# Optimization experiments

Hardware: AMD Instinct MI355X
Metric: run time of the kernel (lower is better)

The kernel has to match this reference:

```python
import jax, jax.numpy as jnp
import numpy as np

N_QUBITS = 4
Q_DEPTH = 6
Q_DELTA = 0.01
INPUT_SIZE = 64
BATCH = 262144


def _ry_gate(theta):
    # RY(theta) = [[cos(t/2), -sin(t/2)], [sin(t/2), cos(t/2)]]; theta scalar or (B,)
    c = jnp.cos(theta / 2)
    s = jnp.sin(theta / 2)
    return jnp.stack([jnp.stack([c, -s], -1), jnp.stack([s, c], -1)], -2)


def _apply_1q(state, gate, wire):
    # state: (B,2,2,2,2); gate: (2,2) shared or (B,2,2) per-sample
    ax = wire + 1
    s = jnp.moveaxis(state, ax, -1)
    if gate.ndim == 2:
        s = jnp.einsum('ij,b...j->b...i', gate, s)
    else:
        s = jnp.einsum('bij,b...j->b...i', gate, s)
    return jnp.moveaxis(s, -1, ax)


def _apply_cnot(state, ctrl, tgt):
    ca, ta = ctrl + 1, tgt + 1
    s0 = jnp.take(state, jnp.array([0]), axis=ca)
    s1 = jnp.take(state, jnp.array([1]), axis=ca)
    s1 = jnp.flip(s1, axis=ta)  # X on target where control=1
    return jnp.concatenate([s0, s1], axis=ca)


def _quantum_net(q_in, q_weights):
    # q_in: (B, 4) per-sample RY angles; q_weights: (Q_DEPTH, 4)
    B = q_in.shape[0]
    # H layer on |0000>: uniform real amplitude 1/4 over all 16 basis states
    state = jnp.full((B,) + (2,) * N_QUBITS, 0.25, dtype=q_in.dtype)
    for w in range(N_QUBITS):
        state = _apply_1q(state, _ry_gate(q_in[:, w]), w)
    for k in range(Q_DEPTH):
        for i in range(0, N_QUBITS - 1, 2):
            state = _apply_cnot(state, i, i + 1)
        for i in range(1, N_QUBITS - 1, 2):
            state = _apply_cnot(state, i, i + 1)
        for w in range(N_QUBITS):
            state = _apply_1q(state, _ry_gate(q_weights[k, w]), w)
    # All gates are real -> real statevector; probs = amp^2
    probs = state * state
    signs = jnp.array([1.0, -1.0], dtype=state.dtype)
    expz = []
    for w in range(N_QUBITS):
        shp = [1] * (N_QUBITS + 1)
        shp[w + 1] = 2
        expz.append(jnp.sum(probs * signs.reshape(shp), axis=tuple(range(1, N_QUBITS + 1))))
    return jnp.stack(expz, axis=-1)  # (B, 4)


def setup_inputs() -> dict:
    key = jax.random.key(0)
    k1, k2, k3, k4, k5, k6 = jax.random.split(key, 6)
    bound_pre = 1.0 / np.sqrt(INPUT_SIZE)
    bound_post = 1.0 / np.sqrt(N_QUBITS)
    return {
        'input_features': jax.random.normal(k1, (BATCH, INPUT_SIZE), dtype=jnp.float32),
        'pre_w': jax.random.uniform(k2, (N_QUBITS, INPUT_SIZE), jnp.float32, -bound_pre, bound_pre),
        'pre_b': jax.random.uniform(k3, (N_QUBITS,), jnp.float32, -bound_pre, bound_pre),
        'q_params': Q_DELTA * jax.random.normal(k4, (Q_DEPTH * N_QUBITS,), dtype=jnp.float32),
        'post_w': jax.random.uniform(k5, (1, N_QUBITS), jnp.float32, -bound_post, bound_post),
        'post_b': jax.random.uniform(k6, (1,), jnp.float32, -bound_post, bound_post),
    }


def reference(input_features, pre_w, pre_b, q_params, post_w, post_b):
    pre_out = input_features @ pre_w.T + pre_b
    q_in = jnp.tanh(pre_out) * (jnp.pi / 2.0)
    q_out = _quantum_net(q_in, q_params.reshape(Q_DEPTH, N_QUBITS))
    return q_out @ post_w.T + post_b  # (B, 1)
```

## Files before the change

### kernel.cpp

```cpp
#include <hip/hip_runtime.h>
#include <math.h>

#define NQ      4
#define QDEPTH  6
#define TPB     128
#define ROWLEN  64
#define LSTRIDE 68

__device__ __forceinline__ float fast_tanh(float x) {
    float e = __expf(2.0f * x);
    float r = __builtin_amdgcn_rcpf(e + 1.0f);
    return fmaf(-2.0f, r, 1.0f);
}

template<int W>
__device__ __forceinline__ void apply_ry(float st[16], float c, float s) {
    constexpr int M = 8 >> W;
#pragma unroll
    for (int i = 0; i < 16; ++i) {
        if ((i & M) == 0) {
            float a0 = st[i];
            float a1 = st[i | M];
            st[i]     = fmaf(c, a0, -(s * a1));
            st[i | M] = fmaf(s, a0,  (c * a1));
        }
    }
}

template<int C, int T>
__device__ __forceinline__ void apply_cnot(float st[16]) {
    constexpr int MC = 8 >> C;
    constexpr int MT = 8 >> T;
#pragma unroll
    for (int i = 0; i < 16; ++i) {
        if ((i & MC) != 0 && (i & MT) == 0) {
            float tmp = st[i];
            st[i] = st[i | MT];
            st[i | MT] = tmp;
        }
    }
}

__global__ __launch_bounds__(TPB, 2) void dqnet_kernel(
    const float* __restrict__ inp,
    const float* __restrict__ pre_w,
    const float* __restrict__ pre_b,
    const float* __restrict__ qp,
    const float* __restrict__ post_w,
    const float* __restrict__ post_b,
    float* __restrict__ out)
{
    __shared__ float tile[TPB * LSTRIDE];
    __shared__ float cw[QDEPTH * NQ];
    __shared__ float sw[QDEPTH * NQ];
    __shared__ float gg[16];

    const int t = threadIdx.x;

    if (t < QDEPTH * NQ) {
        float h = 0.5f * qp[t];
        cw[t] = cosf(h);
        sw[t] = sinf(h);
    } else if (t >= 32 && t < 48) {
        int i = t - 32;
        float v = 0.0f;
#pragma unroll
        for (int w = 0; w < NQ; ++w) {
            float p = post_w[w];
            v += ((i >> (3 - w)) & 1) ? -p : p;
        }
        gg[i] = v;
    }

    const float4* in4 = (const float4*)(inp + (size_t)blockIdx.x * (TPB * ROWLEN));
#pragma unroll
    for (int j = 0; j < 16; ++j) {
        int f = j * TPB + t;
        float4 v = in4[f];
        int s  = f >> 4;
        int c4 = f & 15;
        *(float4*)&tile[s * LSTRIDE + 4 * c4] = v;
    }
    __syncthreads();

    float acc0 = pre_b[0], acc1 = pre_b[1], acc2 = pre_b[2], acc3 = pre_b[3];
    const float4* pw4 = (const float4*)pre_w;
#pragma unroll
    for (int i4 = 0; i4 < 16; ++i4) {
        float4 x  = *(const float4*)&tile[t * LSTRIDE + 4 * i4];
        float4 w0 = pw4[i4];
        float4 w1 = pw4[16 + i4];
        float4 w2 = pw4[32 + i4];
        float4 w3 = pw4[48 + i4];
        acc0 = fmaf(x.x, w0.x, acc0); acc0 = fmaf(x.y, w0.y, acc0);
        acc0 = fmaf(x.z, w0.z, acc0); acc0 = fmaf(x.w, w0.w, acc0);
        acc1 = fmaf(x.x, w1.x, acc1); acc1 = fmaf(x.y, w1.y, acc1);
        acc1 = fmaf(x.z, w1.z, acc1); acc1 = fmaf(x.w, w1.w, acc1);
        acc2 = fmaf(x.x, w2.x, acc2); acc2 = fmaf(x.y, w2.y, acc2);
        acc2 = fmaf(x.z, w2.z, acc2); acc2 = fmaf(x.w, w2.w, acc2);
        acc3 = fmaf(x.x, w3.x, acc3); acc3 = fmaf(x.y, w3.y, acc3);
        acc3 = fmaf(x.z, w3.z, acc3); acc3 = fmaf(x.w, w3.w, acc3);
    }

    const float QK = 0.78539816339744831f;
    float h0 = fast_tanh(acc0) * QK;
    float h1 = fast_tanh(acc1) * QK;
    float h2 = fast_tanh(acc2) * QK;
    float h3 = fast_tanh(acc3) * QK;
    float c0 = __cosf(h0), s0 = __sinf(h0);
    float c1 = __cosf(h1), s1 = __sinf(h1);
    float c2 = __cosf(h2), s2 = __sinf(h2);
    float c3 = __cosf(h3), s3 = __sinf(h3);

    const float R = 0.70710678118654752f;
    float u0 = (c0 - s0) * R, v0 = (c0 + s0) * R;
    float u1 = (c1 - s1) * R, v1 = (c1 + s1) * R;
    float u2 = (c2 - s2) * R, v2 = (c2 + s2) * R;
    float u3 = (c3 - s3) * R, v3 = (c3 + s3) * R;

    float p00 = u0 * u1, p01 = u0 * v1, p10 = v0 * u1, p11 = v0 * v1;
    float q00 = u2 * u3, q01 = u2 * v3, q10 = v2 * u3, q11 = v2 * v3;

    float st[16];
    st[ 0] = p00 * q00; st[ 1] = p00 * q01; st[ 2] = p00 * q10; st[ 3] = p00 * q11;
    st[ 4] = p01 * q00; st[ 5] = p01 * q01; st[ 6] = p01 * q10; st[ 7] = p01 * q11;
    st[ 8] = p10 * q00; st[ 9] = p10 * q01; st[10] = p10 * q10; st[11] = p10 * q11;
    st[12] = p11 * q00; st[13] = p11 * q01; st[14] = p11 * q10; st[15] = p11 * q11;

#pragma unroll
    for (int k = 0; k < QDEPTH; ++k) {
        apply_cnot<0, 1>(st);
        apply_cnot<2, 3>(st);
        apply_cnot<1, 2>(st);
        apply_ry<0>(st, cw[k * 4 + 0], sw[k * 4 + 0]);
        apply_ry<1>(st, cw[k * 4 + 1], sw[k * 4 + 1]);
        apply_ry<2>(st, cw[k * 4 + 2], sw[k * 4 + 2]);
        apply_ry<3>(st, cw[k * 4 + 3], sw[k * 4 + 3]);
    }

    float r = post_b[0];
#pragma unroll
    for (int i = 0; i < 16; ++i)
        r = fmaf(st[i] * st[i], gg[i], r);

    out[(size_t)blockIdx.x * TPB + t] = r;
}

extern "C" void kernel_launch(void* const* d_in, const int* in_sizes, int n_in,
                              void* d_out, int out_size, void* d_ws, size_t ws_size,
                              hipStream_t stream) {
    const float* inp    = (const float*)d_in[0];
    const float* pre_w  = (const float*)d_in[1];
    const float* pre_b  = (const float*)d_in[2];
    const float* qp     = (const float*)d_in[3];
    const float* post_w = (const float*)d_in[4];
    const float* post_b = (const float*)d_in[5];
    float* out = (float*)d_out;

    int n = in_sizes[0] / ROWLEN;
    int grid = n / TPB;
    dqnet_kernel<<<grid, TPB, 0, stream>>>(inp, pre_w, pre_b, qp, post_w, post_b, out);
}
```

Baseline: 103.9 us.

## Load input rows directly from global memory instead of staging through LDS

Drops the shared-memory tile that staged each block's input rows. Each thread now reads its own 256-byte row with float4 loads straight from global memory. Block size doubles to 256 and the launch bound asks for 4 blocks per CU, and the weight cos/sin moves to fast intrinsics. The aim is to remove LDS traffic and free the LDS limit on occupancy, at the cost of strided, uncoalesced per-thread loads across a wavefront that depend on cache-line reuse.

```diff
diff --git a/kernel.cpp b/kernel.cpp
--- a/kernel.cpp
+++ b/kernel.cpp
@@ -3,9 +3,8 @@
 
 #define NQ      4
 #define QDEPTH  6
-#define TPB     128
+#define TPB     256
 #define ROWLEN  64
-#define LSTRIDE 68
 
 __device__ __forceinline__ float fast_tanh(float x) {
     float e = __expf(2.0f * x);
@@ -41,7 +40,7 @@
     }
 }
 
-__global__ __launch_bounds__(TPB, 2) void dqnet_kernel(
+__global__ __launch_bounds__(TPB, 4) void dqnet_kernel(
     const float* __restrict__ inp,
     const float* __restrict__ pre_w,
     const float* __restrict__ pre_b,
@@ -50,7 +49,6 @@
     const float* __restrict__ post_b,
     float* __restrict__ out)
 {
-    __shared__ float tile[TPB * LSTRIDE];
     __shared__ float cw[QDEPTH * NQ];
     __shared__ float sw[QDEPTH * NQ];
     __shared__ float gg[16];
@@ -59,8 +57,8 @@
 
     if (t < QDEPTH * NQ) {
         float h = 0.5f * qp[t];
-        cw[t] = cosf(h);
-        sw[t] = sinf(h);
+        cw[t] = __cosf(h);
+        sw[t] = __sinf(h);
     } else if (t >= 32 && t < 48) {
         int i = t - 32;
         float v = 0.0f;
@@ -71,27 +69,20 @@
         }
         gg[i] = v;
     }
-
-    const float4* in4 = (const float4*)(inp + (size_t)blockIdx.x * (TPB * ROWLEN));
-#pragma unroll
-    for (int j = 0; j < 16; ++j) {
-        int f = j * TPB + t;
-        float4 v = in4[f];
-        int s  = f >> 4;
-        int c4 = f & 15;
-        *(float4*)&tile[s * LSTRIDE + 4 * c4] = v;
-    }
     __syncthreads();
 
+    const size_t row = (size_t)blockIdx.x * TPB + t;
+    const float4* rp  = (const float4*)(inp + row * ROWLEN);
+    const float4* pw4 = (const float4*)pre_w;
+
     float acc0 = pre_b[0], acc1 = pre_b[1], acc2 = pre_b[2], acc3 = pre_b[3];
-    const float4* pw4 = (const float4*)pre_w;
 #pragma unroll
-    for (int i4 = 0; i4 < 16; ++i4) {
-        float4 x  = *(const float4*)&tile[t * LSTRIDE + 4 * i4];
-        float4 w0 = pw4[i4];
-        float4 w1 = pw4[16 + i4];
-        float4 w2 = pw4[32 + i4];
-        float4 w3 = pw4[48 + i4];
+    for (int i = 0; i < 16; ++i) {
+        float4 x  = rp[i];
+        float4 w0 = pw4[i];
+        float4 w1 = pw4[16 + i];
+        float4 w2 = pw4[32 + i];
+        float4 w3 = pw4[48 + i];
         acc0 = fmaf(x.x, w0.x, acc0); acc0 = fmaf(x.y, w0.y, acc0);
         acc0 = fmaf(x.z, w0.z, acc0); acc0 = fmaf(x.w, w0.w, acc0);
         acc1 = fmaf(x.x, w1.x, acc1); acc1 = fmaf(x.y, w1.y, acc1);
@@ -143,7 +134,7 @@
     for (int i = 0; i < 16; ++i)
         r = fmaf(st[i] * st[i], gg[i], r);
 
-    out[(size_t)blockIdx.x * TPB + t] = r;
+    out[row] = r;
 }
 
 extern "C" void kernel_launch(void* const* d_in, const int* in_sizes, int n_in,
```

Measured after the change: 104.8 us. About the same (+0.9%).
